# Kernel optimization log

Hardware: AMD Instinct MI355X
Metric: run time of the kernel (lower is better)

## Reference

```python
import jax, jax.numpy as jnp
import numpy as np

B, N, P, DIM, H = 8, 1024, 77, 1024, 16
HD = DIM // H
LN_EPS = 1e-5


def setup_inputs() -> dict:
    key = jax.random.key(0)
    ks = jax.random.split(key, 8)
    s = 0.02  # weight init scale
    return {
        "x": jax.random.normal(ks[0], (B, N, DIM), jnp.float32),
        "x_text": jax.random.normal(ks[1], (B, P, DIM), jnp.float32),
        "Wq": jax.random.normal(ks[2], (DIM, DIM), jnp.float32) * s,
        "Wk": jax.random.normal(ks[3], (DIM, DIM), jnp.float32) * s,
        "Wv": jax.random.normal(ks[4], (DIM, DIM), jnp.float32) * s,
        "gate": jax.random.normal(ks[5], (1, H, 1, 1), jnp.float32) * 0.5,
        "ln_g": jnp.ones((DIM,), jnp.float32),
        "ln_b": jnp.zeros((DIM,), jnp.float32),
        "Wp": jax.random.normal(ks[6], (DIM, DIM), jnp.float32) * s,
        "bp": jnp.zeros((DIM,), jnp.float32),
    }


def reference(x, x_text, Wq, Wk, Wv, gate, ln_g, ln_b, Wp, bp):
    b, n, c = x.shape
    h = gate.shape[1]
    # subln projections; prefix text tokens are concatenated onto k/v (not q)
    q = x @ Wq.T                                             # [B,N,C]
    k = jnp.concatenate([x_text @ Wk.T, x @ Wk.T], axis=1)   # [B,P+N,C]
    v = jnp.concatenate([x_text @ Wv.T, x @ Wv.T], axis=1)   # [B,P+N,C]
    kv = k.shape[1]
    q = q.reshape(b, n, h, -1).transpose(0, 2, 1, 3)         # [B,H,N,d]
    k = k.reshape(b, kv, h, -1).transpose(0, 2, 1, 3)        # [B,H,K,d]
    v = v.reshape(b, kv, h, -1).transpose(0, 2, 1, 3)        # [B,H,K,d]
    d = q.shape[-1]
    scores = jnp.einsum('bhnd,bhkd->bhnk', q, k) / jnp.sqrt(jnp.float32(d))
    # gated split softmax: first key column is softmaxed alone (== 1) and gated
    first = jnp.tanh(gate) * jnp.ones_like(scores[..., :1])  # [B,H,N,1]
    rest = jax.nn.softmax(scores[..., 1:], axis=-1)          # [B,H,N,K-1]
    attn = jnp.concatenate([first, rest], axis=-1)           # [B,H,N,K]
    out = jnp.einsum('bhnk,bhkd->bhnd', attn, v)             # AV reduce
    out = out.transpose(0, 2, 1, 3).reshape(b, n, -1)        # [B,N,C]
    # original casts to bfloat16 then back to LN weight dtype
    out = out.astype(jnp.bfloat16).astype(jnp.float32)
    mu = jnp.mean(out, axis=-1, keepdims=True)
    var = jnp.var(out, axis=-1, keepdims=True)
    out = (out - mu) / jnp.sqrt(var + LN_EPS) * ln_g + ln_b
    return out @ Wp.T + bp
```

## Files before the change

### kernel.cpp

```cpp
#include <hip/hip_runtime.h>
#include <stdint.h>

#define DIM   1024
#define NB    8
#define NSEQ  1024
#define NP    77
#define NH    16
#define NKVR  1104
#define KVP   1104
#define NTILE 18
#define PLD   68

typedef short          bf16x8 __attribute__((ext_vector_type(8)));
typedef float          f32x4  __attribute__((ext_vector_type(4)));
typedef unsigned short u16x8  __attribute__((ext_vector_type(8)));
typedef unsigned short u16x4  __attribute__((ext_vector_type(4)));
typedef unsigned int   u32x4  __attribute__((ext_vector_type(4)));

__device__ __forceinline__ float bf2f(unsigned short h) {
  return __uint_as_float(((unsigned int)h) << 16);
}
__device__ __forceinline__ unsigned short f2bf(float f) {
  unsigned int u = __float_as_uint(f);
  unsigned int r = u + 0x7FFFu + ((u >> 16) & 1u);
  return (unsigned short)(r >> 16);
}
__device__ __forceinline__ unsigned int cvt_pk_bf16(float lo, float hi) {
  unsigned int r;
  asm volatile("v_cvt_pk_bf16_f32 %0, %1, %2" : "=v"(r) : "v"(lo), "v"(hi));
  return r;
}

__global__ __launch_bounds__(256) void cast_kernel(const float* __restrict__ in,
                                                   unsigned short* __restrict__ out,
                                                   int n4) {
  int i = blockIdx.x * 256 + threadIdx.x;
  if (i >= n4) return;
  float4 v = reinterpret_cast<const float4*>(in)[i];
  u16x4 o;
  o[0] = f2bf(v.x); o[1] = f2bf(v.y); o[2] = f2bf(v.z); o[3] = f2bf(v.w);
  reinterpret_cast<u16x4*>(out)[i] = o;
}

__global__ __launch_bounds__(256) void cast_x_kernel(const float* __restrict__ in,
                                                     unsigned short* __restrict__ xkv) {
  int i = blockIdx.x * 256 + threadIdx.x;
  if (i >= (NB * NSEQ * DIM) / 4) return;
  const int e    = i * 4;
  const int row  = e >> 10;
  const int cin  = e & 1023;
  const int batch = row >> 10;
  const int r     = row & 1023;
  float4 v = *reinterpret_cast<const float4*>(in + (size_t)e);
  u16x4 o;
  o[0] = f2bf(v.x); o[1] = f2bf(v.y); o[2] = f2bf(v.z); o[3] = f2bf(v.w);
  *reinterpret_cast<u16x4*>(xkv + (size_t)(batch * NKVR + 80 + r) * DIM + cin) = o;
}

__global__ __launch_bounds__(256) void cast_xt_kernel(const float* __restrict__ in,
                                                      unsigned short* __restrict__ xkv) {
  int i = blockIdx.x * 256 + threadIdx.x;
  if (i >= (NB * NP * DIM) / 4) return;
  const int e    = i * 4;
  const int row  = e >> 10;
  const int cin  = e & 1023;
  const int batch = row / NP;
  const int r     = row - batch * NP;
  float4 v = *reinterpret_cast<const float4*>(in + (size_t)e);
  u16x4 o;
  o[0] = f2bf(v.x); o[1] = f2bf(v.y); o[2] = f2bf(v.z); o[3] = f2bf(v.w);
  *reinterpret_cast<u16x4*>(xkv + (size_t)(batch * NKVR + r) * DIM + cin) = o;
}

__global__ __launch_bounds__(256) void zero_hole_kernel(unsigned short* __restrict__ xkv) {
  int i = blockIdx.x * 256 + threadIdx.x;
  if (i >= (NB * 3 * DIM) / 4) return;
  const int e    = i * 4;
  const int row  = e >> 10;
  const int cin  = e & 1023;
  const int batch = row / 3;
  const int hr    = row - batch * 3;
  u16x4 z = {0, 0, 0, 0};
  *reinterpret_cast<u16x4*>(xkv + (size_t)(batch * NKVR + 77 + hr) * DIM + cin) = z;
}

__device__ __forceinline__ void gload_lds16(const void* g, void* l) {
  __builtin_amdgcn_global_load_lds(
      (const __attribute__((address_space(1))) void*)g,
      (__attribute__((address_space(3))) void*)l, 16, 0, 0);
}

__global__ __launch_bounds__(256) void gemm_qkv(
    const unsigned short* __restrict__ A, const unsigned short* __restrict__ B,
    unsigned short* __restrict__ Qo, unsigned short* __restrict__ Ko,
    unsigned short* __restrict__ Vto) {
  __shared__ __align__(16) unsigned short As[128 * 32];
  __shared__ __align__(16) unsigned short Bs[128 * 32];
  const int id   = blockIdx.x;
  const int sid  = (id & 7) * 207 + (id >> 3);
  const int bx   = sid / 24;
  const int by   = sid - bx * 24;
  const int m0   = bx * 128;
  const int n0   = by * 128;
  const int t    = threadIdx.x;
  const int w    = t >> 6;
  const int lane = t & 63;
  const int wr   = w >> 1, wc = w & 1;
  const int lr   = lane & 15;
  const int k0   = (lane >> 4) * 8;

  f32x4 acc[4][4];
#pragma unroll
  for (int i = 0; i < 4; ++i)
#pragma unroll
    for (int j = 0; j < 4; ++j) acc[i][j] = f32x4{0.f, 0.f, 0.f, 0.f};

  for (int kt = 0; kt < 32; ++kt) {
#pragma unroll
    for (int p = 0; p < 2; ++p) {
      const int c   = p * 256 + t;
      const int row = c >> 2;
      const int cid = c & 3;
      gload_lds16(A + (size_t)(m0 + row) * DIM + kt * 32 + cid * 8,
                  (char*)As + p * 4096 + w * 1024);
      gload_lds16(B + (size_t)(n0 + row) * DIM + kt * 32 + cid * 8,
                  (char*)Bs + p * 4096 + w * 1024);
    }
    __syncthreads();
    bf16x8 af[4], bfr[4];
#pragma unroll
    for (int mi = 0; mi < 4; ++mi)
      af[mi] = *reinterpret_cast<const bf16x8*>(As + (wr * 64 + mi * 16 + lr) * 32 + k0);
#pragma unroll
    for (int ni = 0; ni < 4; ++ni)
      bfr[ni] = *reinterpret_cast<const bf16x8*>(Bs + (wc * 64 + ni * 16 + lr) * 32 + k0);
#pragma unroll
    for (int mi = 0; mi < 4; ++mi)
#pragma unroll
      for (int ni = 0; ni < 4; ++ni)
        acc[mi][ni] = __builtin_amdgcn_mfma_f32_16x16x32_bf16(af[mi], bfr[ni], acc[mi][ni], 0, 0, 0);
    __syncthreads();
  }

  const int rq  = lane >> 4;
  const int seg = n0 >> 10;
  if (seg == 0) {
#pragma unroll
    for (int mi = 0; mi < 4; ++mi) {
#pragma unroll
      for (int i = 0; i < 4; ++i) {
        const int m     = m0 + wr * 64 + mi * 16 + rq * 4 + i;
        const int batch = m / NKVR;
        const int kv    = m - batch * NKVR;
        if (kv < 80) continue;
        const size_t qrow = (size_t)batch * NSEQ + (kv - 80);
#pragma unroll
        for (int ni = 0; ni < 4; ++ni) {
          const int col = n0 + wc * 64 + ni * 16 + lr;
          Qo[qrow * DIM + col] = f2bf(acc[mi][ni][i]);
        }
      }
    }
  } else if (seg == 1) {
#pragma unroll
    for (int mi = 0; mi < 4; ++mi) {
#pragma unroll
      for (int i = 0; i < 4; ++i) {
        const int m = m0 + wr * 64 + mi * 16 + rq * 4 + i;
#pragma unroll
        for (int ni = 0; ni < 4; ++ni) {
          const int col = n0 + wc * 64 + ni * 16 + lr - 1024;
          Ko[(size_t)m * DIM + col] = f2bf(acc[mi][ni][i]);
        }
      }
    }
  } else {
#pragma unroll
    for (int mi = 0; mi < 4; ++mi) {
      const int mb    = m0 + wr * 64 + mi * 16 + rq * 4;
      const int batch = mb / NKVR;
      const int kv    = mb - batch * NKVR;
#pragma unroll
      for (int ni = 0; ni < 4; ++ni) {
        const int col = n0 + wc * 64 + ni * 16 + lr - 2048;
        const int hh = col >> 6, dd = col & 63;
        u16x4 o;
        o[0] = f2bf(acc[mi][ni][0]); o[1] = f2bf(acc[mi][ni][1]);
        o[2] = f2bf(acc[mi][ni][2]); o[3] = f2bf(acc[mi][ni][3]);
        *reinterpret_cast<u16x4*>(Vto +
            ((size_t)((batch * NH + hh) * 64 + dd)) * KVP + kv) = o;
      }
    }
  }
}

__global__ __launch_bounds__(256) void gemm_out(
    const unsigned short* __restrict__ A, const unsigned short* __restrict__ B,
    float* __restrict__ C, const float* __restrict__ bias) {
  __shared__ __align__(16) unsigned short As[128 * 32];
  __shared__ __align__(16) unsigned short Bs[128 * 32];
  const int t    = threadIdx.x;
  const int w    = t >> 6;
  const int lane = t & 63;
  const int m0   = blockIdx.x * 128;
  const int n0   = blockIdx.y * 128;
  const int wr   = w >> 1, wc = w & 1;
  const int lr   = lane & 15;
  const int k0   = (lane >> 4) * 8;

  f32x4 acc[4][4];
#pragma unroll
  for (int i = 0; i < 4; ++i)
#pragma unroll
    for (int j = 0; j < 4; ++j) acc[i][j] = f32x4{0.f, 0.f, 0.f, 0.f};

  for (int kt = 0; kt < 32; ++kt) {
#pragma unroll
    for (int p = 0; p < 2; ++p) {
      const int c   = p * 256 + t;
      const int row = c >> 2;
      const int cid = c & 3;
      gload_lds16(A + (size_t)(m0 + row) * DIM + kt * 32 + cid * 8,
                  (char*)As + p * 4096 + w * 1024);
      gload_lds16(B + (size_t)(n0 + row) * DIM + kt * 32 + cid * 8,
                  (char*)Bs + p * 4096 + w * 1024);
    }
    __syncthreads();
    bf16x8 af[4], bfr[4];
#pragma unroll
    for (int mi = 0; mi < 4; ++mi)
      af[mi] = *reinterpret_cast<const bf16x8*>(As + (wr * 64 + mi * 16 + lr) * 32 + k0);
#pragma unroll
    for (int ni = 0; ni < 4; ++ni)
      bfr[ni] = *reinterpret_cast<const bf16x8*>(Bs + (wc * 64 + ni * 16 + lr) * 32 + k0);
#pragma unroll
    for (int mi = 0; mi < 4; ++mi)
#pragma unroll
      for (int ni = 0; ni < 4; ++ni)
        acc[mi][ni] = __builtin_amdgcn_mfma_f32_16x16x32_bf16(af[mi], bfr[ni], acc[mi][ni], 0, 0, 0);
    __syncthreads();
  }

  const int rq = lane >> 4;
#pragma unroll
  for (int mi = 0; mi < 4; ++mi) {
#pragma unroll
    for (int i = 0; i < 4; ++i) {
      const int m = m0 + wr * 64 + mi * 16 + rq * 4 + i;
#pragma unroll
      for (int ni = 0; ni < 4; ++ni) {
        const int col = n0 + wc * 64 + ni * 16 + lr;
        C[(size_t)m * DIM + col] = acc[mi][ni][i] + bias[col];
      }
    }
  }
}

__global__ __launch_bounds__(256) void attn_mfma(
    const unsigned short* __restrict__ Q, const unsigned short* __restrict__ K,
    const unsigned short* __restrict__ Vt, const float* __restrict__ gate,
    unsigned short* __restrict__ O) {
  const int wid  = threadIdx.x >> 6;
  const int lane = threadIdx.x & 63;
  const int lr   = lane & 15;
  const int lg   = lane >> 4;
  const int bh   = blockIdx.x;
  const int b    = bh >> 4;
  const int h    = bh & 15;
  const int q0   = blockIdx.y * 128 + wid * 32;

  __shared__ __align__(16) float p_lds[4][32 * PLD];

  bf16x8 aq[2][2];
#pragma unroll
  for (int mi = 0; mi < 2; ++mi)
#pragma unroll
    for (int kf = 0; kf < 2; ++kf)
      aq[mi][kf] = *reinterpret_cast<const bf16x8*>(
          Q + ((size_t)(b * NSEQ + q0 + mi * 16 + lr)) * DIM + h * 64 + kf * 32 + lg * 8);

  f32x4 accO[2][4];
#pragma unroll
  for (int mi = 0; mi < 2; ++mi)
#pragma unroll
    for (int n = 0; n < 4; ++n) accO[mi][n] = f32x4{0.f, 0.f, 0.f, 0.f};
  float lsum[2][4];
#pragma unroll
  for (int mi = 0; mi < 2; ++mi)
#pragma unroll
    for (int r = 0; r < 4; ++r) lsum[mi][r] = 0.f;

  const unsigned short* Kbase  = K  + ((size_t)b * NKVR) * DIM + h * 64 + lg * 8;
  const unsigned short* Vtbase = Vt + ((size_t)((b * NH + h) * 64)) * KVP;
  float* pl = p_lds[wid];

  for (int tkv = 0; tkv < NTILE; ++tkv) {
    const int kv0 = tkv * 64;
    bf16x8 bk[4][2];
#pragma unroll
    for (int ni = 0; ni < 4; ++ni) {
      int kvn = kv0 + ni * 16 + lr;
      kvn = kvn < (NKVR - 1) ? kvn : (NKVR - 1);
      const unsigned short* kr = Kbase + (size_t)kvn * DIM;
#pragma unroll
      for (int kf = 0; kf < 2; ++kf)
        bk[ni][kf] = *reinterpret_cast<const bf16x8*>(kr + kf * 32);
    }
    f32x4 S[2][4];
#pragma unroll
    for (int mi = 0; mi < 2; ++mi)
#pragma unroll
      for (int ni = 0; ni < 4; ++ni) S[mi][ni] = f32x4{0.f, 0.f, 0.f, 0.f};
#pragma unroll
    for (int ni = 0; ni < 4; ++ni)
#pragma unroll
      for (int kf = 0; kf < 2; ++kf)
#pragma unroll
        for (int mi = 0; mi < 2; ++mi)
          S[mi][ni] = __builtin_amdgcn_mfma_f32_16x16x32_bf16(aq[mi][kf], bk[ni][kf], S[mi][ni], 0, 0, 0);
    bf16x8 bv[4][2];
#pragma unroll
    for (int n = 0; n < 4; ++n) {
      const unsigned short* vr = Vtbase + (size_t)(n * 16 + lr) * KVP;
#pragma unroll
      for (int kf = 0; kf < 2; ++kf) {
        int kvb = kv0 + kf * 32 + lg * 8;
        kvb = kvb < (KVP - 8) ? kvb : (KVP - 8);
        bv[n][kf] = *reinterpret_cast<const bf16x8*>(vr + kvb);
      }
    }
    if (tkv < 2 || tkv == NTILE - 1) {
#pragma unroll
      for (int ni = 0; ni < 4; ++ni) {
        const int gk = kv0 + ni * 16 + lr;
        const bool bad = (gk == 0) || ((unsigned)(gk - 77) < 3u) || (gk >= NKVR);
        if (bad) {
#pragma unroll
          for (int mi = 0; mi < 2; ++mi)
#pragma unroll
            for (int r = 0; r < 4; ++r) S[mi][ni][r] = -1.0e30f;
        }
      }
    }
#pragma unroll
    for (int mi = 0; mi < 2; ++mi) {
#pragma unroll
      for (int ni = 0; ni < 4; ++ni) {
#pragma unroll
        for (int r = 0; r < 4; ++r)
          S[mi][ni][r] = __expf(0.125f * S[mi][ni][r]);
      }
#pragma unroll
      for (int r = 0; r < 4; ++r)
        lsum[mi][r] += (S[mi][0][r] + S[mi][1][r]) + (S[mi][2][r] + S[mi][3][r]);
#pragma unroll
      for (int ni = 0; ni < 4; ++ni) {
        float* pw = pl + (size_t)(mi * 16 + lg * 4) * PLD + ni * 16 + lr;
        pw[0 * PLD] = S[mi][ni][0];
        pw[1 * PLD] = S[mi][ni][1];
        pw[2 * PLD] = S[mi][ni][2];
        pw[3 * PLD] = S[mi][ni][3];
      }
    }
    bf16x8 pa[2][2];
#pragma unroll
    for (int mi = 0; mi < 2; ++mi) {
#pragma unroll
      for (int kf = 0; kf < 2; ++kf) {
        const float* pr = pl + (size_t)(mi * 16 + lr) * PLD + kf * 32 + lg * 8;
        const float4 pa0 = *reinterpret_cast<const float4*>(pr);
        const float4 pa1 = *reinterpret_cast<const float4*>(pr + 4);
        u32x4 pk;
        pk[0] = cvt_pk_bf16(pa0.x, pa0.y);
        pk[1] = cvt_pk_bf16(pa0.z, pa0.w);
        pk[2] = cvt_pk_bf16(pa1.x, pa1.y);
        pk[3] = cvt_pk_bf16(pa1.z, pa1.w);
        pa[mi][kf] = __builtin_bit_cast(bf16x8, pk);
      }
    }
#pragma unroll
    for (int n = 0; n < 4; ++n)
#pragma unroll
      for (int kf = 0; kf < 2; ++kf)
#pragma unroll
        for (int mi = 0; mi < 2; ++mi)
          accO[mi][n] = __builtin_amdgcn_mfma_f32_16x16x32_bf16(pa[mi][kf], bv[n][kf], accO[mi][n], 0, 0, 0);
  }

#pragma unroll
  for (int mi = 0; mi < 2; ++mi) {
#pragma unroll
    for (int r = 0; r < 4; ++r) {
      float s = lsum[mi][r];
      s += __shfl_xor(s, 1);
      s += __shfl_xor(s, 2);
      s += __shfl_xor(s, 4);
      s += __shfl_xor(s, 8);
      lsum[mi][r] = 1.f / s;
    }
  }
  const float gv = tanhf(gate[h]);
#pragma unroll
  for (int mi = 0; mi < 2; ++mi) {
#pragma unroll
    for (int n = 0; n < 4; ++n) {
      const float v0 = bf2f(Vtbase[(size_t)(n * 16 + lr) * KVP]);
#pragma unroll
      for (int r = 0; r < 4; ++r) {
        const float o = accO[mi][n][r] * lsum[mi][r] + gv * v0;
        const int q = q0 + mi * 16 + lg * 4 + r;
        O[((size_t)(b * NSEQ + q)) * DIM + h * 64 + n * 16 + lr] = f2bf(o);
      }
    }
  }
}

__global__ __launch_bounds__(256) void ln_kernel(const unsigned short* __restrict__ in,
                                                 const float* __restrict__ g,
                                                 const float* __restrict__ beta,
                                                 unsigned short* __restrict__ out) {
  const int row = blockIdx.x;
  const int t   = threadIdx.x;
  const u16x4 hv = *reinterpret_cast<const u16x4*>(in + (size_t)row * DIM + t * 4);
  const float v0 = bf2f(hv[0]), v1 = bf2f(hv[1]), v2 = bf2f(hv[2]), v3 = bf2f(hv[3]);
  float sum = v0 + v1 + v2 + v3;
  float sq  = v0 * v0 + v1 * v1 + v2 * v2 + v3 * v3;
  for (int off = 32; off; off >>= 1) {
    sum += __shfl_xor(sum, off);
    sq  += __shfl_xor(sq, off);
  }
  __shared__ float red[8];
  if ((t & 63) == 0) { red[t >> 6] = sum; red[4 + (t >> 6)] = sq; }
  __syncthreads();
  sum = red[0] + red[1] + red[2] + red[3];
  sq  = red[4] + red[5] + red[6] + red[7];
  const float mu  = sum * (1.f / DIM);
  const float var = sq * (1.f / DIM) - mu * mu;
  const float rs  = 1.f / sqrtf(var + 1e-5f);
  const float4 gv = *reinterpret_cast<const float4*>(g + t * 4);
  const float4 bv = *reinterpret_cast<const float4*>(beta + t * 4);
  u16x4 o;
  o[0] = f2bf((v0 - mu) * rs * gv.x + bv.x);
  o[1] = f2bf((v1 - mu) * rs * gv.y + bv.y);
  o[2] = f2bf((v2 - mu) * rs * gv.z + bv.z);
  o[3] = f2bf((v3 - mu) * rs * gv.w + bv.w);
  *reinterpret_cast<u16x4*>(out + (size_t)row * DIM + t * 4) = o;
}

extern "C" void kernel_launch(void* const* d_in, const int* in_sizes, int n_in,
                              void* d_out, int out_size, void* d_ws, size_t ws_size,
                              hipStream_t stream) {
  const float* x    = (const float*)d_in[0];
  const float* xt   = (const float*)d_in[1];
  const float* Wq   = (const float*)d_in[2];
  const float* Wk   = (const float*)d_in[3];
  const float* Wv   = (const float*)d_in[4];
  const float* gate = (const float*)d_in[5];
  const float* lng  = (const float*)d_in[6];
  const float* lnbt = (const float*)d_in[7];
  const float* Wp   = (const float*)d_in[8];
  const float* bp   = (const float*)d_in[9];

  char* ws = (char*)d_ws;
  unsigned short* xkvb = (unsigned short*)(ws + 0);
  unsigned short* Wqkv = (unsigned short*)(ws + 18087936);
  unsigned short* Qb   = (unsigned short*)(ws + 24379392);
  unsigned short* Kb   = (unsigned short*)(ws + 41156608);
  unsigned short* Vtb  = (unsigned short*)(ws + 59244544);
  unsigned short* attnb = xkvb;
  unsigned short* lnob  = Qb;
  unsigned short* Wpb   = Wqkv;

  cast_x_kernel<<<dim3((NB * NSEQ * DIM / 4 + 255) / 256), 256, 0, stream>>>(x, xkvb);
  cast_xt_kernel<<<dim3((NB * NP * DIM / 4 + 255) / 256), 256, 0, stream>>>(xt, xkvb);
  zero_hole_kernel<<<dim3((NB * 3 * DIM / 4 + 255) / 256), 256, 0, stream>>>(xkvb);
  const int w4 = DIM * DIM / 4;
  cast_kernel<<<dim3((w4 + 255) / 256), 256, 0, stream>>>(Wq, Wqkv, w4);
  cast_kernel<<<dim3((w4 + 255) / 256), 256, 0, stream>>>(Wk, Wqkv + DIM * DIM, w4);
  cast_kernel<<<dim3((w4 + 255) / 256), 256, 0, stream>>>(Wv, Wqkv + 2 * DIM * DIM, w4);

  gemm_qkv<<<dim3(69 * 24), 256, 0, stream>>>(xkvb, Wqkv, Qb, Kb, Vtb);

  attn_mfma<<<dim3(128, 8), 256, 0, stream>>>(Qb, Kb, Vtb, gate, attnb);

  cast_kernel<<<dim3((w4 + 255) / 256), 256, 0, stream>>>(Wp, Wpb, w4);
  ln_kernel<<<dim3(NB * NSEQ), 256, 0, stream>>>(attnb, lng, lnbt, lnob);
  gemm_out<<<dim3(64, 8), 256, 0, stream>>>(lnob, Wpb, (float*)d_out, bp);
}
```

Baseline: 246.4 us.

## Double-buffer LDS tiles in QKV and output GEMMs to overlap loads with MFMA

After: 251.6 us. 1.02x slower.

```diff
diff --git a/kernel.cpp b/kernel.cpp
--- a/kernel.cpp
+++ b/kernel.cpp
@@ -94,8 +94,8 @@
     const unsigned short* __restrict__ A, const unsigned short* __restrict__ B,
     unsigned short* __restrict__ Qo, unsigned short* __restrict__ Ko,
     unsigned short* __restrict__ Vto) {
-  __shared__ __align__(16) unsigned short As[128 * 32];
-  __shared__ __align__(16) unsigned short Bs[128 * 32];
+  __shared__ __align__(16) unsigned short As[2 * 128 * 32];
+  __shared__ __align__(16) unsigned short Bs[2 * 128 * 32];
   const int id   = blockIdx.x;
   const int sid  = (id & 7) * 207 + (id >> 3);
   const int bx   = sid / 24;
@@ -115,31 +115,47 @@
 #pragma unroll
     for (int j = 0; j < 4; ++j) acc[i][j] = f32x4{0.f, 0.f, 0.f, 0.f};
 
-  for (int kt = 0; kt < 32; ++kt) {
+  auto stage = [&](int bufi, int kt) {
 #pragma unroll
     for (int p = 0; p < 2; ++p) {
       const int c   = p * 256 + t;
       const int row = c >> 2;
       const int cid = c & 3;
       gload_lds16(A + (size_t)(m0 + row) * DIM + kt * 32 + cid * 8,
-                  (char*)As + p * 4096 + w * 1024);
+                  (char*)As + bufi * 8192 + p * 4096 + w * 1024);
       gload_lds16(B + (size_t)(n0 + row) * DIM + kt * 32 + cid * 8,
-                  (char*)Bs + p * 4096 + w * 1024);
-    }
-    __syncthreads();
+                  (char*)Bs + bufi * 8192 + p * 4096 + w * 1024);
+    }
+  };
+
+  stage(0, 0);
+  int cur = 0;
+  for (int kt = 0; kt < 32; ++kt) {
+    if (kt < 31) {
+      stage(cur ^ 1, kt + 1);
+      asm volatile("s_waitcnt vmcnt(4)" ::: "memory");
+    } else {
+      asm volatile("s_waitcnt vmcnt(0)" ::: "memory");
+    }
+    __builtin_amdgcn_s_barrier();
+    __builtin_amdgcn_sched_barrier(0);
+    const unsigned short* Ac = As + cur * 4096;
+    const unsigned short* Bc = Bs + cur * 4096;
     bf16x8 af[4], bfr[4];
 #pragma unroll
     for (int mi = 0; mi < 4; ++mi)
-      af[mi] = *reinterpret_cast<const bf16x8*>(As + (wr * 64 + mi * 16 + lr) * 32 + k0);
+      af[mi] = *reinterpret_cast<const bf16x8*>(Ac + (wr * 64 + mi * 16 + lr) * 32 + k0);
 #pragma unroll
     for (int ni = 0; ni < 4; ++ni)
-      bfr[ni] = *reinterpret_cast<const bf16x8*>(Bs + (wc * 64 + ni * 16 + lr) * 32 + k0);
+      bfr[ni] = *reinterpret_cast<const bf16x8*>(Bc + (wc * 64 + ni * 16 + lr) * 32 + k0);
 #pragma unroll
     for (int mi = 0; mi < 4; ++mi)
 #pragma unroll
       for (int ni = 0; ni < 4; ++ni)
         acc[mi][ni] = __builtin_amdgcn_mfma_f32_16x16x32_bf16(af[mi], bfr[ni], acc[mi][ni], 0, 0, 0);
-    __syncthreads();
+    __builtin_amdgcn_sched_barrier(0);
+    __builtin_amdgcn_s_barrier();
+    cur ^= 1;
   }
 
   const int rq  = lane >> 4;
@@ -197,8 +213,8 @@
 __global__ __launch_bounds__(256) void gemm_out(
     const unsigned short* __restrict__ A, const unsigned short* __restrict__ B,
     float* __restrict__ C, const float* __restrict__ bias) {
-  __shared__ __align__(16) unsigned short As[128 * 32];
-  __shared__ __align__(16) unsigned short Bs[128 * 32];
+  __shared__ __align__(16) unsigned short As[2 * 128 * 32];
+  __shared__ __align__(16) unsigned short Bs[2 * 128 * 32];
   const int t    = threadIdx.x;
   const int w    = t >> 6;
   const int lane = t & 63;
@@ -214,31 +230,47 @@
 #pragma unroll
     for (int j = 0; j < 4; ++j) acc[i][j] = f32x4{0.f, 0.f, 0.f, 0.f};
 
-  for (int kt = 0; kt < 32; ++kt) {
+  auto stage = [&](int bufi, int kt) {
 #pragma unroll
     for (int p = 0; p < 2; ++p) {
       const int c   = p * 256 + t;
       const int row = c >> 2;
       const int cid = c & 3;
       gload_lds16(A + (size_t)(m0 + row) * DIM + kt * 32 + cid * 8,
-                  (char*)As + p * 4096 + w * 1024);
+                  (char*)As + bufi * 8192 + p * 4096 + w * 1024);
       gload_lds16(B + (size_t)(n0 + row) * DIM + kt * 32 + cid * 8,
-                  (char*)Bs + p * 4096 + w * 1024);
-    }
-    __syncthreads();
+                  (char*)Bs + bufi * 8192 + p * 4096 + w * 1024);
+    }
+  };
+
+  stage(0, 0);
+  int cur = 0;
+  for (int kt = 0; kt < 32; ++kt) {
+    if (kt < 31) {
+      stage(cur ^ 1, kt + 1);
+      asm volatile("s_waitcnt vmcnt(4)" ::: "memory");
+    } else {
+      asm volatile("s_waitcnt vmcnt(0)" ::: "memory");
+    }
+    __builtin_amdgcn_s_barrier();
+    __builtin_amdgcn_sched_barrier(0);
+    const unsigned short* Ac = As + cur * 4096;
+    const unsigned short* Bc = Bs + cur * 4096;
     bf16x8 af[4], bfr[4];
 #pragma unroll
     for (int mi = 0; mi < 4; ++mi)
-      af[mi] = *reinterpret_cast<const bf16x8*>(As + (wr * 64 + mi * 16 + lr) * 32 + k0);
+      af[mi] = *reinterpret_cast<const bf16x8*>(Ac + (wr * 64 + mi * 16 + lr) * 32 + k0);
 #pragma unroll
     for (int ni = 0; ni < 4; ++ni)
-      bfr[ni] = *reinterpret_cast<const bf16x8*>(Bs + (wc * 64 + ni * 16 + lr) * 32 + k0);
+      bfr[ni] = *reinterpret_cast<const bf16x8*>(Bc + (wc * 64 + ni * 16 + lr) * 32 + k0);
 #pragma unroll
     for (int mi = 0; mi < 4; ++mi)
 #pragma unroll
       for (int ni = 0; ni < 4; ++ni)
         acc[mi][ni] = __builtin_amdgcn_mfma_f32_16x16x32_bf16(af[mi], bfr[ni], acc[mi][ni], 0, 0, 0);
-    __syncthreads();
+    __builtin_amdgcn_sched_barrier(0);
+    __builtin_amdgcn_s_barrier();
+    cur ^= 1;
   }
 
   const int rq = lane >> 4;
```
